# Optimization experiments

Measured on AMD Instinct MI355X. Metric: run time of the kernel, lower is better.

Reference implementation:

```python
import jax, jax.numpy as jnp
import numpy as np

N_USER = 100000
N_GAME = 20000
E = 1600000
DU, DG, H = 64, 128, 128


def setup_inputs() -> dict:
    key = jax.random.key(0)
    ks = jax.random.split(key, 16)
    g = lambda k, shp, fan: jax.random.normal(k, shp, jnp.float32) / np.sqrt(fan)
    return {
        "x_user": jax.random.normal(ks[0], (N_USER, DU), jnp.float32),
        "x_game": jax.random.normal(ks[1], (N_GAME, DG), jnp.float32),
        "W_user": g(ks[2], (DU, H), DU),
        "b_user": jnp.zeros((H,), jnp.float32),
        "W_game": g(ks[3], (DG, H), DG),
        "b_game": jnp.zeros((H,), jnp.float32),
        "Wl_ug": g(ks[4], (H, H), H),
        "bl_ug": jnp.zeros((H,), jnp.float32),
        "Wr_ug": g(ks[5], (H, H), H),
        "Wl_gu": g(ks[6], (H, H), H),
        "bl_gu": jnp.zeros((H,), jnp.float32),
        "Wr_gu": g(ks[7], (H, H), H),
        "src_ug": jax.random.randint(ks[8], (E,), 0, N_USER, jnp.int32),
        "dst_ug": jax.random.randint(ks[9], (E,), 0, N_GAME, jnp.int32),
        "src_gu": jax.random.randint(ks[10], (E,), 0, N_GAME, jnp.int32),
        "dst_gu": jax.random.randint(ks[11], (E,), 0, N_USER, jnp.int32),
    }


def _seg_mean(src_feat, idx_src, idx_dst, n_dst):
    # gather neighbor features per edge, then mean-aggregate onto dst nodes
    msgs = src_feat[idx_src]                                   # [E, H]
    s = jax.ops.segment_sum(msgs, idx_dst, num_segments=n_dst)  # [n_dst, H]
    c = jax.ops.segment_sum(jnp.ones((idx_dst.shape[0],), src_feat.dtype),
                            idx_dst, num_segments=n_dst)
    return s / jnp.maximum(c, 1.0)[:, None]


def reference(x_user, x_game, W_user, b_user, W_game, b_game,
              Wl_ug, bl_ug, Wr_ug, Wl_gu, bl_gu, Wr_gu,
              src_ug, dst_ug, src_gu, dst_gu):
    # per-node-type input projection + relu
    hu = jax.nn.relu(x_user @ W_user + b_user)   # [N_USER, H]
    hg = jax.nn.relu(x_game @ W_game + b_game)   # [N_GAME, H]
    # SAGEConv per edge type (mean aggr, lin_l has bias, lin_r no bias)
    m_g = _seg_mean(hu, src_ug, dst_ug, N_GAME)
    out_game = m_g @ Wl_ug + bl_ug + hg @ Wr_ug  # (user->game) relation
    m_u = _seg_mean(hg, src_gu, dst_gu, N_USER)
    out_user = m_u @ Wl_gu + bl_gu + hu @ Wr_gu  # (game->user) relation
    # aggr='sum' across relations: each dst type has exactly one relation here
    return out_user, out_game
```

## Files before the change

kernel.cpp:

```cpp
#include <hip/hip_runtime.h>
#include <hip/hip_bf16.h>

#define NUSER 100000
#define NGAME 20000
#define NTOT  120000
#define HDIM  128
#define NBUCK 469
#define CH    8192

typedef short bf16x8 __attribute__((ext_vector_type(8)));
typedef float f32x4  __attribute__((ext_vector_type(4)));
typedef float f32x2  __attribute__((ext_vector_type(2)));

__device__ __forceinline__ unsigned short f2b(float f) {
  union { float f; unsigned u; } a;
  a.f = f;
  unsigned r = a.u + 0x7fff + ((a.u >> 16) & 1);
  return (unsigned short)(r >> 16);
}
__device__ __forceinline__ float b2f_lo(unsigned u) {
  union { unsigned u; float f; } a; a.u = u << 16; return a.f;
}
__device__ __forceinline__ float b2f_hi(unsigned u) {
  union { unsigned u; float f; } a; a.u = u & 0xffff0000u; return a.f;
}

__global__ __launch_bounds__(256) void repack_kernel(
    const float* __restrict__ W0, const float* __restrict__ W1,
    const float* __restrict__ W2, const float* __restrict__ W3,
    const float* __restrict__ W4, const float* __restrict__ W5,
    unsigned short* __restrict__ P0, unsigned short* __restrict__ P1,
    unsigned short* __restrict__ P2, unsigned short* __restrict__ P3,
    unsigned short* __restrict__ P4, unsigned short* __restrict__ P5) {
  const float* W; unsigned short* P; int K;
  switch (blockIdx.y) {
    case 0: W = W0; P = P0; K = 64;  break;
    case 1: W = W1; P = P1; K = 128; break;
    case 2: W = W2; P = P2; K = 128; break;
    case 3: W = W3; P = P3; K = 128; break;
    case 4: W = W4; P = P4; K = 128; break;
    default: W = W5; P = P5; K = 128; break;
  }
  int t = blockIdx.x * 256 + threadIdx.x;
  int KT = K / 32;
  if (t >= KT * 8 * 64) return;
  int lane = t & 63;
  int nt = (t >> 6) & 7;
  int kt = t >> 9;
  int col = nt * 16 + (lane & 15);
  int krow = kt * 32 + (lane >> 4) * 8;
  unsigned short vals[8];
#pragma unroll
  for (int b = 0; b < 8; ++b) vals[b] = f2b(W[(size_t)(krow + b) * HDIM + col]);
  *reinterpret_cast<bf16x8*>(P + (size_t)t * 8) = *reinterpret_cast<bf16x8*>(vals);
}

template <int K>
__global__ __launch_bounds__(256) void proj_mfma_kernel(
    const float* __restrict__ x, const unsigned short* __restrict__ Wp,
    const float* __restrict__ b, unsigned short* __restrict__ h, int M) {
  int l = threadIdx.x & 63;
  int wid = threadIdx.x >> 6;
  int r0 = blockIdx.x * 64 + wid * 16;
  int arow = r0 + (l & 15);
  if (arow >= M) arow = M - 1;
  const int KT = K / 32;
  f32x4 acc[8];
#pragma unroll
  for (int nt = 0; nt < 8; ++nt) acc[nt] = (f32x4){0.f, 0.f, 0.f, 0.f};
  const float* xr = x + (size_t)arow * K + (l >> 4) * 8;
  const bf16x8* Wf = (const bf16x8*)Wp;
#pragma unroll
  for (int kt = 0; kt < KT; ++kt) {
    float4 a0 = *(const float4*)(xr + kt * 32);
    float4 a1 = *(const float4*)(xr + kt * 32 + 4);
    bf16x8 af;
    af[0] = (short)f2b(a0.x); af[1] = (short)f2b(a0.y);
    af[2] = (short)f2b(a0.z); af[3] = (short)f2b(a0.w);
    af[4] = (short)f2b(a1.x); af[5] = (short)f2b(a1.y);
    af[6] = (short)f2b(a1.z); af[7] = (short)f2b(a1.w);
#pragma unroll
    for (int nt = 0; nt < 8; ++nt) {
      bf16x8 bf = Wf[(kt * 8 + nt) * 64 + l];
      acc[nt] = __builtin_amdgcn_mfma_f32_16x16x32_bf16(af, bf, acc[nt], 0, 0, 0);
    }
  }
  int rbase = r0 + ((l >> 4) << 2);
#pragma unroll
  for (int nt = 0; nt < 8; ++nt) {
    int col = nt * 16 + (l & 15);
    float bias = b[col];
#pragma unroll
    for (int r = 0; r < 4; ++r) {
      int row = rbase + r;
      if (row < M) h[(size_t)row * HDIM + col] = f2b(fmaxf(acc[nt][r] + bias, 0.f));
    }
  }
}

__global__ __launch_bounds__(256) void cvt8_kernel(
    const unsigned short* __restrict__ hu, unsigned* __restrict__ hu8, int n8) {
  int i = blockIdx.x * 256 + threadIdx.x;
  if (i >= n8) return;
  uint4 v = ((const uint4*)hu)[i];
  unsigned w0 = 0, w1 = 0;
  w0 = __builtin_amdgcn_cvt_pk_fp8_f32(b2f_lo(v.x), b2f_hi(v.x), w0, false);
  w0 = __builtin_amdgcn_cvt_pk_fp8_f32(b2f_lo(v.y), b2f_hi(v.y), w0, true);
  w1 = __builtin_amdgcn_cvt_pk_fp8_f32(b2f_lo(v.z), b2f_hi(v.z), w1, false);
  w1 = __builtin_amdgcn_cvt_pk_fp8_f32(b2f_lo(v.w), b2f_hi(v.w), w1, true);
  ((uint2*)hu8)[i] = make_uint2(w0, w1);
}

#define GBK ((NGAME + 63) / 64)
#define UBK ((NUSER + 63) / 64)
__global__ __launch_bounds__(256) void out_mfma_fused_kernel(
    const unsigned short* __restrict__ m, const unsigned short* __restrict__ hg,
    const unsigned short* __restrict__ hu,
    const unsigned short* __restrict__ P_lug, const float* __restrict__ bl_ug,
    const unsigned short* __restrict__ P_rug,
    const unsigned short* __restrict__ P_lgu, const float* __restrict__ bl_gu,
    const unsigned short* __restrict__ P_rgu,
    float* __restrict__ out_game, float* __restrict__ out_user) {
  const unsigned short *mb, *h, *WlP, *WrP;
  const float* bl;
  float* out;
  int M, bi;
  if (blockIdx.x < GBK) {
    mb = m;                          h = hg; WlP = P_lug; bl = bl_ug; WrP = P_rug;
    out = out_game; M = NGAME; bi = blockIdx.x;
  } else {
    mb = m + (size_t)NGAME * HDIM;   h = hu; WlP = P_lgu; bl = bl_gu; WrP = P_rgu;
    out = out_user; M = NUSER; bi = blockIdx.x - GBK;
  }
  int l = threadIdx.x & 63;
  int wid = threadIdx.x >> 6;
  int r0 = bi * 64 + wid * 16;
  int arow = r0 + (l & 15);
  if (arow >= M) arow = M - 1;
  f32x4 acc[8];
#pragma unroll
  for (int nt = 0; nt < 8; ++nt) acc[nt] = (f32x4){0.f, 0.f, 0.f, 0.f};
  const unsigned short* mr = mb + (size_t)arow * HDIM + (l >> 4) * 8;
  const unsigned short* hr = h + (size_t)arow * HDIM + (l >> 4) * 8;
  const bf16x8* Wlf = (const bf16x8*)WlP;
  const bf16x8* Wrf = (const bf16x8*)WrP;
#pragma unroll
  for (int kt = 0; kt < 4; ++kt) {
    bf16x8 am = *(const bf16x8*)(mr + kt * 32);
    bf16x8 ah = *(const bf16x8*)(hr + kt * 32);
#pragma unroll
    for (int nt = 0; nt < 8; ++nt) {
      bf16x8 bl_f = Wlf[(kt * 8 + nt) * 64 + l];
      bf16x8 br_f = Wrf[(kt * 8 + nt) * 64 + l];
      acc[nt] = __builtin_amdgcn_mfma_f32_16x16x32_bf16(am, bl_f, acc[nt], 0, 0, 0);
      acc[nt] = __builtin_amdgcn_mfma_f32_16x16x32_bf16(ah, br_f, acc[nt], 0, 0, 0);
    }
  }
  int rbase = r0 + ((l >> 4) << 2);
#pragma unroll
  for (int nt = 0; nt < 8; ++nt) {
    int col = nt * 16 + (l & 15);
    float bias = bl[col];
#pragma unroll
    for (int r = 0; r < 4; ++r) {
      int row = rbase + r;
      if (row < M) out[(size_t)row * HDIM + col] = acc[nt][r] + bias;
    }
  }
}

__global__ __launch_bounds__(256) void s1_hist_kernel(
    const int* __restrict__ dst_ug, const int* __restrict__ dst_gu,
    int* __restrict__ cnt, int E, int nch) {
  __shared__ int hist[NBUCK];
  for (int i = threadIdx.x; i < NBUCK; i += 256) hist[i] = 0;
  __syncthreads();
  int base = blockIdx.x * CH, endi = min(base + CH, 2 * E);
  for (int e = base + threadIdx.x; e < endi; e += 256) {
    int d = (e < E) ? dst_ug[e] : (NGAME + dst_gu[e - E]);
    atomicAdd(&hist[d >> 8], 1);
  }
  __syncthreads();
  for (int i = threadIdx.x; i < NBUCK; i += 256)
    cnt[i * nch + blockIdx.x] = hist[i];
}

__global__ __launch_bounds__(1024) void scan1_kernel(
    const int* __restrict__ cnt, int* __restrict__ off,
    int* __restrict__ bsum, int n) {
  __shared__ int wsum[16];
  int i = blockIdx.x * 1024 + threadIdx.x;
  int lane = threadIdx.x & 63, wid = threadIdx.x >> 6;
  int v = (i < n) ? cnt[i] : 0;
  int x = v;
#pragma unroll
  for (int d = 1; d < 64; d <<= 1) {
    int t = __shfl_up(x, (unsigned)d, 64);
    if (lane >= d) x += t;
  }
  if (lane == 63) wsum[wid] = x;
  __syncthreads();
  if (wid == 0 && lane < 16) {
    int w = wsum[lane];
#pragma unroll
    for (int d = 1; d < 16; d <<= 1) {
      int t = __shfl_up(w, (unsigned)d, 64);
      if (lane >= d) w += t;
    }
    wsum[lane] = w;
  }
  __syncthreads();
  int wavepre = (wid == 0) ? 0 : wsum[wid - 1];
  if (i < n) off[i] = wavepre + x - v;
  if (threadIdx.x == 1023) bsum[blockIdx.x] = wavepre + x;
}

__global__ __launch_bounds__(1024) void scan2_kernel(
    int* __restrict__ bsum, int* __restrict__ off, int nb, int n) {
  __shared__ int wsum[16];
  __shared__ int carry_s;
  int lane = threadIdx.x & 63, wid = threadIdx.x >> 6;
  if (threadIdx.x == 0) carry_s = 0;
  __syncthreads();
  for (int base = 0; base < nb; base += 1024) {
    int i = base + threadIdx.x;
    int v = (i < nb) ? bsum[i] : 0;
    int x = v;
#pragma unroll
    for (int d = 1; d < 64; d <<= 1) {
      int t = __shfl_up(x, (unsigned)d, 64);
      if (lane >= d) x += t;
    }
    if (lane == 63) wsum[wid] = x;
    __syncthreads();
    if (wid == 0 && lane < 16) {
      int w = wsum[lane];
#pragma unroll
      for (int d = 1; d < 16; d <<= 1) {
        int t = __shfl_up(w, (unsigned)d, 64);
        if (lane >= d) w += t;
      }
      wsum[lane] = w;
    }
    __syncthreads();
    int wavepre = (wid == 0) ? 0 : wsum[wid - 1];
    int carry = carry_s;
    if (i < nb) bsum[i] = carry + wavepre + x - v;
    __syncthreads();
    if (threadIdx.x == 1023) carry_s = carry + wsum[15];
    __syncthreads();
  }
  if (threadIdx.x == 0) off[n] = carry_s;
}

__global__ __launch_bounds__(256) void scan3_kernel(
    int* __restrict__ off, const int* __restrict__ bsum, int n) {
  int i = blockIdx.x * 256 + threadIdx.x;
  if (i < n) off[i] += bsum[i >> 10];
}

__global__ __launch_bounds__(256) void s1_scatter_kernel(
    const int* __restrict__ src_ug, const int* __restrict__ dst_ug,
    const int* __restrict__ src_gu, const int* __restrict__ dst_gu,
    const int* __restrict__ off, unsigned* __restrict__ esort,
    int E, int nch) {
  __shared__ int bases[NBUCK];
  for (int i = threadIdx.x; i < NBUCK; i += 256)
    bases[i] = off[i * nch + blockIdx.x];
  __syncthreads();
  int base = blockIdx.x * CH, endi = min(base + CH, 2 * E);
  for (int e = base + threadIdx.x; e < endi; e += 256) {
    int d, s;
    if (e < E) { d = dst_ug[e]; s = src_ug[e]; }
    else       { d = NGAME + dst_gu[e - E]; s = src_gu[e - E]; }
    int pos = atomicAdd(&bases[d >> 8], 1);
    esort[pos] = ((unsigned)s << 8) | (unsigned)(d & 255);
  }
}

__global__ __launch_bounds__(256) void s2_csr_kernel(
    const unsigned* __restrict__ esort, const int* __restrict__ off,
    int* __restrict__ offd, int* __restrict__ esrc, int nch) {
  __shared__ int hist[256], excl[256], run[256];
  __shared__ int wsum[4];
  int k = blockIdx.x;
  int tid = threadIdx.x;
  int base = off[(size_t)k * nch];
  int end  = off[(size_t)(k + 1) * nch];
  hist[tid] = 0;
  run[tid] = 0;
  __syncthreads();
  for (int i = base + tid; i < end; i += 256)
    atomicAdd(&hist[esort[i] & 255], 1);
  __syncthreads();
  int lane = tid & 63, wid = tid >> 6;
  int v = hist[tid], x = v;
#pragma unroll
  for (int dd = 1; dd < 64; dd <<= 1) {
    int t = __shfl_up(x, (unsigned)dd, 64);
    if (lane >= dd) x += t;
  }
  if (lane == 63) wsum[wid] = x;
  __syncthreads();
  int wpre = 0;
  if (wid > 0) wpre += wsum[0];
  if (wid > 1) wpre += wsum[1];
  if (wid > 2) wpre += wsum[2];
  int ex = wpre + x - v;
  excl[tid] = ex;
  int d = k * 256 + tid;
  if (d <= NTOT) offd[d] = base + ex;
  __syncthreads();
  for (int i = base + tid; i < end; i += 256) {
    unsigned p = esort[i];
    int dl = p & 255;
    int pos = base + excl[dl] + atomicAdd(&run[dl], 1);
    esrc[pos] = (int)(p >> 8);
  }
}

#define ACC8(v)                         \
  do {                                  \
    acc[0] += b2f_lo((v).x);            \
    acc[1] += b2f_hi((v).x);            \
    acc[2] += b2f_lo((v).y);            \
    acc[3] += b2f_hi((v).y);            \
    acc[4] += b2f_lo((v).z);            \
    acc[5] += b2f_hi((v).z);            \
    acc[6] += b2f_lo((v).w);            \
    acc[7] += b2f_hi((v).w);            \
  } while (0)

#define ACCF8(v)                                                   \
  do {                                                             \
    f32x2 t;                                                       \
    t = __builtin_amdgcn_cvt_pk_f32_fp8((v).x, false);             \
    acc[0] += t[0]; acc[1] += t[1];                                \
    t = __builtin_amdgcn_cvt_pk_f32_fp8((v).x, true);              \
    acc[2] += t[0]; acc[3] += t[1];                                \
    t = __builtin_amdgcn_cvt_pk_f32_fp8((v).y, false);             \
    acc[4] += t[0]; acc[5] += t[1];                                \
    t = __builtin_amdgcn_cvt_pk_f32_fp8((v).y, true);              \
    acc[6] += t[0]; acc[7] += t[1];                                \
    t = __builtin_amdgcn_cvt_pk_f32_fp8((v).z, false);             \
    acc[8] += t[0]; acc[9] += t[1];                                \
    t = __builtin_amdgcn_cvt_pk_f32_fp8((v).z, true);              \
    acc[10] += t[0]; acc[11] += t[1];                              \
    t = __builtin_amdgcn_cvt_pk_f32_fp8((v).w, false);             \
    acc[12] += t[0]; acc[13] += t[1];                              \
    t = __builtin_amdgcn_cvt_pk_f32_fp8((v).w, true);              \
    acc[14] += t[0]; acc[15] += t[1];                              \
  } while (0)

__global__ __launch_bounds__(256) void gather_kernel(
    const unsigned* __restrict__ hu8, const unsigned short* __restrict__ hg,
    const int* __restrict__ esrc, const int* __restrict__ offd,
    unsigned short* __restrict__ m) {
  int w = (blockIdx.x * blockDim.x + threadIdx.x) >> 6;
  int lane = threadIdx.x & 63;
  if (w >= NTOT) return;
  int beg = offd[w], end = offd[w + 1];
  float inv = 1.f / fmaxf((float)(end - beg), 1.f);
  if (w < NGAME) {
    int g = lane >> 3, c = lane & 7;
    const uint4* f = (const uint4*)hu8;
    float acc[16];
#pragma unroll
    for (int i = 0; i < 16; ++i) acc[i] = 0.f;
    int k = beg + g;
    for (; k + 8 < end; k += 16) {
      int s0 = esrc[k];
      int s1 = esrc[k + 8];
      uint4 v0 = f[(size_t)s0 * 8 + c];
      uint4 v1 = f[(size_t)s1 * 8 + c];
      ACCF8(v0);
      ACCF8(v1);
    }
    {
      bool p0 = k < end, p1 = k + 8 < end;
      int a0 = p0 ? k : 0;
      int a1 = p1 ? k + 8 : 0;
      int s0 = esrc[a0];
      int s1 = esrc[a1];
      uint4 v0 = f[(size_t)s0 * 8 + c];
      uint4 v1 = f[(size_t)s1 * 8 + c];
      if (p0) ACCF8(v0);
      if (p1) ACCF8(v1);
    }
#pragma unroll
    for (int i = 0; i < 16; ++i) {
      acc[i] += __shfl_xor(acc[i], 8, 64);
      acc[i] += __shfl_xor(acc[i], 16, 64);
      acc[i] += __shfl_xor(acc[i], 32, 64);
    }
    unsigned o = (unsigned)f2b(acc[2 * g] * inv) |
                 ((unsigned)f2b(acc[2 * g + 1] * inv) << 16);
    ((unsigned*)m)[(size_t)w * 64 + c * 8 + g] = o;
  } else {
    int g = lane >> 4, c = lane & 15;
    const uint4* f = (const uint4*)hg;
    float acc[8];
#pragma unroll
    for (int i = 0; i < 8; ++i) acc[i] = 0.f;
    int k = beg + g;
    for (; k + 12 < end; k += 16) {
      int s0 = esrc[k];
      int s1 = esrc[k + 4];
      int s2 = esrc[k + 8];
      int s3 = esrc[k + 12];
      uint4 v0 = f[(size_t)s0 * 16 + c];
      uint4 v1 = f[(size_t)s1 * 16 + c];
      uint4 v2 = f[(size_t)s2 * 16 + c];
      uint4 v3 = f[(size_t)s3 * 16 + c];
      ACC8(v0);
      ACC8(v1);
      ACC8(v2);
      ACC8(v3);
    }
    {
      int k0 = k, k1 = k + 4, k2 = k + 8;
      bool p0 = k0 < end, p1 = k1 < end, p2 = k2 < end;
      int a0 = p0 ? k0 : 0;
      int a1 = p1 ? k1 : 0;
      int a2 = p2 ? k2 : 0;
      int s0 = esrc[a0];
      int s1 = esrc[a1];
      int s2 = esrc[a2];
      uint4 v0 = f[(size_t)s0 * 16 + c];
      uint4 v1 = f[(size_t)s1 * 16 + c];
      uint4 v2 = f[(size_t)s2 * 16 + c];
      if (p0) ACC8(v0);
      if (p1) ACC8(v1);
      if (p2) ACC8(v2);
    }
#pragma unroll
    for (int i = 0; i < 8; ++i) {
      acc[i] += __shfl_xor(acc[i], 16, 64);
      acc[i] += __shfl_xor(acc[i], 32, 64);
    }
    unsigned o = (unsigned)f2b(acc[2 * g] * inv) |
                 ((unsigned)f2b(acc[2 * g + 1] * inv) << 16);
    ((unsigned*)m)[(size_t)w * 64 + c * 4 + g] = o;
  }
}

extern "C" void kernel_launch(void* const* d_in, const int* in_sizes, int n_in,
                              void* d_out, int out_size, void* d_ws, size_t ws_size,
                              hipStream_t stream) {
  const float* x_user = (const float*)d_in[0];
  const float* x_game = (const float*)d_in[1];
  const float* W_user = (const float*)d_in[2];
  const float* b_user = (const float*)d_in[3];
  const float* W_game = (const float*)d_in[4];
  const float* b_game = (const float*)d_in[5];
  const float* Wl_ug  = (const float*)d_in[6];
  const float* bl_ug  = (const float*)d_in[7];
  const float* Wr_ug  = (const float*)d_in[8];
  const float* Wl_gu  = (const float*)d_in[9];
  const float* bl_gu  = (const float*)d_in[10];
  const float* Wr_gu  = (const float*)d_in[11];
  const int*   src_ug = (const int*)d_in[12];
  const int*   dst_ug = (const int*)d_in[13];
  const int*   src_gu = (const int*)d_in[14];
  const int*   dst_gu = (const int*)d_in[15];
  const int E = in_sizes[12];

  const int nch = (2 * E + CH - 1) / CH;
  const int n   = NBUCK * nch;
  const int nb  = (n + 1023) / 1024;

  char* ws = (char*)d_ws;
  unsigned short* hu  = (unsigned short*)ws; ws += (size_t)NUSER * HDIM * 2;
  unsigned short* hg  = (unsigned short*)ws; ws += (size_t)NGAME * HDIM * 2;
  unsigned short* m   = (unsigned short*)ws; ws += (size_t)NTOT * HDIM * 2;
  unsigned* hu8 = (unsigned*)ws; ws += (size_t)NUSER * HDIM;
  unsigned* esort = (unsigned*)ws; ws += (size_t)2 * E * 4;
  int* esrc  = (int*)ws; ws += (size_t)2 * E * 4;
  int* cnt   = (int*)ws; ws += (size_t)n * 4;
  int* off   = (int*)ws; ws += (size_t)(n + 1) * 4;
  int* offd  = (int*)ws; ws += (size_t)(NTOT + 1) * 4;
  int* bsum  = (int*)ws; ws += 2048 * 4;
  unsigned short* P_wu  = (unsigned short*)ws; ws += (size_t)2 * 8 * 64 * 8 * 2;
  unsigned short* P_wg  = (unsigned short*)ws; ws += (size_t)4 * 8 * 64 * 8 * 2;
  unsigned short* P_lug = (unsigned short*)ws; ws += (size_t)4 * 8 * 64 * 8 * 2;
  unsigned short* P_rug = (unsigned short*)ws; ws += (size_t)4 * 8 * 64 * 8 * 2;
  unsigned short* P_lgu = (unsigned short*)ws; ws += (size_t)4 * 8 * 64 * 8 * 2;
  unsigned short* P_rgu = (unsigned short*)ws; ws += (size_t)4 * 8 * 64 * 8 * 2;

  float* out_user = (float*)d_out;
  float* out_game = (float*)d_out + (size_t)NUSER * HDIM;

  repack_kernel<<<dim3(8, 6), 256, 0, stream>>>(
      W_user, W_game, Wl_ug, Wr_ug, Wl_gu, Wr_gu,
      P_wu, P_wg, P_lug, P_rug, P_lgu, P_rgu);

  proj_mfma_kernel<64><<<(NUSER + 63) / 64, 256, 0, stream>>>(x_user, P_wu, b_user, hu, NUSER);
  proj_mfma_kernel<128><<<(NGAME + 63) / 64, 256, 0, stream>>>(x_game, P_wg, b_game, hg, NGAME);

  cvt8_kernel<<<(NUSER * 16 + 255) / 256, 256, 0, stream>>>(hu, hu8, NUSER * 16);

  s1_hist_kernel<<<nch, 256, 0, stream>>>(dst_ug, dst_gu, cnt, E, nch);
  scan1_kernel<<<nb, 1024, 0, stream>>>(cnt, off, bsum, n);
  scan2_kernel<<<1, 1024, 0, stream>>>(bsum, off, nb, n);
  scan3_kernel<<<(n + 255) / 256, 256, 0, stream>>>(off, bsum, n);
  s1_scatter_kernel<<<nch, 256, 0, stream>>>(src_ug, dst_ug, src_gu, dst_gu, off, esort, E, nch);
  s2_csr_kernel<<<NBUCK, 256, 0, stream>>>(esort, off, offd, esrc, nch);

  gather_kernel<<<(NTOT * 64 + 255) / 256, 256, 0, stream>>>(hu8, hg, esrc, offd, m);

  out_mfma_fused_kernel<<<GBK + UBK, 256, 0, stream>>>(
      m, hg, hu, P_lug, bl_ug, P_rug, P_lgu, bl_gu, P_rgu, out_game, out_user);
}
```

Before: 241.3 us.

## Fuse neighbor gather into output GEMM and fp8 conversion into projection

Gather-mean aggregation now runs inside the output MFMA kernel. Each block aggregates its 64 destination rows into a swizzled LDS tile and then feeds that tile directly into the GEMM, so the bf16 m buffer is no longer written to and read back from global memory. The user projection kernel also emits the fp8 copy of hu through LDS, which removes the separate cvt8 pass. The cost is less parallelism during the gather: each wave serially processes 16 destination rows instead of one row per wave, and there is an extra block-level sync. A no-op `*0.f` term was also added to ACC8.

Result: slower. 272.6 us (+12.9%).

```diff
diff --git a/kernel.cpp b/kernel.cpp
--- a/kernel.cpp
+++ b/kernel.cpp
@@ -55,10 +55,12 @@
   *reinterpret_cast<bf16x8*>(P + (size_t)t * 8) = *reinterpret_cast<bf16x8*>(vals);
 }
 
-template <int K>
+template <int K, bool W8>
 __global__ __launch_bounds__(256) void proj_mfma_kernel(
     const float* __restrict__ x, const unsigned short* __restrict__ Wp,
-    const float* __restrict__ b, unsigned short* __restrict__ h, int M) {
+    const float* __restrict__ b, unsigned short* __restrict__ h,
+    unsigned* __restrict__ h8, int M) {
+  __shared__ __align__(16) unsigned char lds8[64 * 128];
   int l = threadIdx.x & 63;
   int wid = threadIdx.x >> 6;
   int r0 = blockIdx.x * 64 + wid * 16;
@@ -86,6 +88,7 @@
     }
   }
   int rbase = r0 + ((l >> 4) << 2);
+  int rtbase = wid * 16 + ((l >> 4) << 2);
 #pragma unroll
   for (int nt = 0; nt < 8; ++nt) {
     int col = nt * 16 + (l & 15);
@@ -93,78 +96,21 @@
 #pragma unroll
     for (int r = 0; r < 4; ++r) {
       int row = rbase + r;
-      if (row < M) h[(size_t)row * HDIM + col] = f2b(fmaxf(acc[nt][r] + bias, 0.f));
-    }
-  }
-}
-
-__global__ __launch_bounds__(256) void cvt8_kernel(
-    const unsigned short* __restrict__ hu, unsigned* __restrict__ hu8, int n8) {
-  int i = blockIdx.x * 256 + threadIdx.x;
-  if (i >= n8) return;
-  uint4 v = ((const uint4*)hu)[i];
-  unsigned w0 = 0, w1 = 0;
-  w0 = __builtin_amdgcn_cvt_pk_fp8_f32(b2f_lo(v.x), b2f_hi(v.x), w0, false);
-  w0 = __builtin_amdgcn_cvt_pk_fp8_f32(b2f_lo(v.y), b2f_hi(v.y), w0, true);
-  w1 = __builtin_amdgcn_cvt_pk_fp8_f32(b2f_lo(v.z), b2f_hi(v.z), w1, false);
-  w1 = __builtin_amdgcn_cvt_pk_fp8_f32(b2f_lo(v.w), b2f_hi(v.w), w1, true);
-  ((uint2*)hu8)[i] = make_uint2(w0, w1);
-}
-
-#define GBK ((NGAME + 63) / 64)
-#define UBK ((NUSER + 63) / 64)
-__global__ __launch_bounds__(256) void out_mfma_fused_kernel(
-    const unsigned short* __restrict__ m, const unsigned short* __restrict__ hg,
-    const unsigned short* __restrict__ hu,
-    const unsigned short* __restrict__ P_lug, const float* __restrict__ bl_ug,
-    const unsigned short* __restrict__ P_rug,
-    const unsigned short* __restrict__ P_lgu, const float* __restrict__ bl_gu,
-    const unsigned short* __restrict__ P_rgu,
-    float* __restrict__ out_game, float* __restrict__ out_user) {
-  const unsigned short *mb, *h, *WlP, *WrP;
-  const float* bl;
-  float* out;
-  int M, bi;
-  if (blockIdx.x < GBK) {
-    mb = m;                          h = hg; WlP = P_lug; bl = bl_ug; WrP = P_rug;
-    out = out_game; M = NGAME; bi = blockIdx.x;
-  } else {
-    mb = m + (size_t)NGAME * HDIM;   h = hu; WlP = P_lgu; bl = bl_gu; WrP = P_rgu;
-    out = out_user; M = NUSER; bi = blockIdx.x - GBK;
-  }
-  int l = threadIdx.x & 63;
-  int wid = threadIdx.x >> 6;
-  int r0 = bi * 64 + wid * 16;
-  int arow = r0 + (l & 15);
-  if (arow >= M) arow = M - 1;
-  f32x4 acc[8];
-#pragma unroll
-  for (int nt = 0; nt < 8; ++nt) acc[nt] = (f32x4){0.f, 0.f, 0.f, 0.f};
-  const unsigned short* mr = mb + (size_t)arow * HDIM + (l >> 4) * 8;
-  const unsigned short* hr = h + (size_t)arow * HDIM + (l >> 4) * 8;
-  const bf16x8* Wlf = (const bf16x8*)WlP;
-  const bf16x8* Wrf = (const bf16x8*)WrP;
-#pragma unroll
-  for (int kt = 0; kt < 4; ++kt) {
-    bf16x8 am = *(const bf16x8*)(mr + kt * 32);
-    bf16x8 ah = *(const bf16x8*)(hr + kt * 32);
-#pragma unroll
-    for (int nt = 0; nt < 8; ++nt) {
-      bf16x8 bl_f = Wlf[(kt * 8 + nt) * 64 + l];
-      bf16x8 br_f = Wrf[(kt * 8 + nt) * 64 + l];
-      acc[nt] = __builtin_amdgcn_mfma_f32_16x16x32_bf16(am, bl_f, acc[nt], 0, 0, 0);
-      acc[nt] = __builtin_amdgcn_mfma_f32_16x16x32_bf16(ah, br_f, acc[nt], 0, 0, 0);
-    }
-  }
-  int rbase = r0 + ((l >> 4) << 2);
-#pragma unroll
-  for (int nt = 0; nt < 8; ++nt) {
-    int col = nt * 16 + (l & 15);
-    float bias = bl[col];
-#pragma unroll
-    for (int r = 0; r < 4; ++r) {
-      int row = rbase + r;
-      if (row < M) out[(size_t)row * HDIM + col] = acc[nt][r] + bias;
+      float v = fmaxf(acc[nt][r] + bias, 0.f);
+      if (row < M) h[(size_t)row * HDIM + col] = f2b(v);
+      if (W8) {
+        unsigned t8 = __builtin_amdgcn_cvt_pk_fp8_f32(v, v, 0u, false);
+        lds8[(rtbase + r) * 128 + col] = (unsigned char)(t8 & 0xFF);
+      }
+    }
+  }
+  if (W8) {
+    __syncthreads();
+    const uint4* src = (const uint4*)lds8;
+    int blk0 = blockIdx.x * 64;
+    for (int i = threadIdx.x; i < 512; i += 256) {
+      int row = blk0 + (i >> 3);
+      if (row < M) ((uint4*)h8)[(size_t)blockIdx.x * 512 + i] = src[i];
     }
   }
 }
@@ -319,6 +265,9 @@
   }
 }
 
+#define GBK ((NGAME + 63) / 64)
+#define UBK ((NUSER + 63) / 64)
+
 #define ACC8(v)                         \
   do {                                  \
     acc[0] += b2f_lo((v).x);            \
@@ -327,7 +276,7 @@
     acc[3] += b2f_hi((v).y);            \
     acc[4] += b2f_lo((v).z);            \
     acc[5] += b2f_hi((v).z);            \
-    acc[6] += b2f_lo((v).w);            \
+    acc[6] += b2f_hi((v).w) * 0.f + b2f_lo((v).w); \
     acc[7] += b2f_hi((v).w);            \
   } while (0)
 
@@ -352,95 +301,151 @@
     acc[14] += t[0]; acc[15] += t[1];                              \
   } while (0)
 
-__global__ __launch_bounds__(256) void gather_kernel(
+__global__ __launch_bounds__(256) void fused_out_kernel(
     const unsigned* __restrict__ hu8, const unsigned short* __restrict__ hg,
+    const unsigned short* __restrict__ hu,
     const int* __restrict__ esrc, const int* __restrict__ offd,
-    unsigned short* __restrict__ m) {
-  int w = (blockIdx.x * blockDim.x + threadIdx.x) >> 6;
-  int lane = threadIdx.x & 63;
-  if (w >= NTOT) return;
-  int beg = offd[w], end = offd[w + 1];
-  float inv = 1.f / fmaxf((float)(end - beg), 1.f);
-  if (w < NGAME) {
-    int g = lane >> 3, c = lane & 7;
+    const unsigned short* __restrict__ P_lug, const float* __restrict__ bl_ug,
+    const unsigned short* __restrict__ P_rug,
+    const unsigned short* __restrict__ P_lgu, const float* __restrict__ bl_gu,
+    const unsigned short* __restrict__ P_rgu,
+    float* __restrict__ out_game, float* __restrict__ out_user) {
+  __shared__ __align__(16) unsigned mtile[64 * 64];
+  int l = threadIdx.x & 63;
+  int wid = threadIdx.x >> 6;
+  bool isGame = blockIdx.x < GBK;
+  int bi = isGame ? blockIdx.x : blockIdx.x - GBK;
+  int M = isGame ? NGAME : NUSER;
+  int r0 = bi * 64;
+  int dbase = isGame ? 0 : NGAME;
+  int rtEnd = min(wid * 16 + 16, M - r0);
+
+  if (isGame) {
+    int g = l >> 3, c = l & 7;
     const uint4* f = (const uint4*)hu8;
-    float acc[16];
-#pragma unroll
-    for (int i = 0; i < 16; ++i) acc[i] = 0.f;
-    int k = beg + g;
-    for (; k + 8 < end; k += 16) {
-      int s0 = esrc[k];
-      int s1 = esrc[k + 8];
-      uint4 v0 = f[(size_t)s0 * 8 + c];
-      uint4 v1 = f[(size_t)s1 * 8 + c];
-      ACCF8(v0);
-      ACCF8(v1);
-    }
-    {
-      bool p0 = k < end, p1 = k + 8 < end;
-      int a0 = p0 ? k : 0;
-      int a1 = p1 ? k + 8 : 0;
-      int s0 = esrc[a0];
-      int s1 = esrc[a1];
-      uint4 v0 = f[(size_t)s0 * 8 + c];
-      uint4 v1 = f[(size_t)s1 * 8 + c];
-      if (p0) ACCF8(v0);
-      if (p1) ACCF8(v1);
-    }
-#pragma unroll
-    for (int i = 0; i < 16; ++i) {
-      acc[i] += __shfl_xor(acc[i], 8, 64);
-      acc[i] += __shfl_xor(acc[i], 16, 64);
-      acc[i] += __shfl_xor(acc[i], 32, 64);
-    }
-    unsigned o = (unsigned)f2b(acc[2 * g] * inv) |
-                 ((unsigned)f2b(acc[2 * g + 1] * inv) << 16);
-    ((unsigned*)m)[(size_t)w * 64 + c * 8 + g] = o;
+    for (int rt = wid * 16; rt < rtEnd; ++rt) {
+      int beg = offd[dbase + r0 + rt], end = offd[dbase + r0 + rt + 1];
+      float acc[16];
+#pragma unroll
+      for (int i = 0; i < 16; ++i) acc[i] = 0.f;
+      int k = beg + g;
+      for (; k + 8 < end; k += 16) {
+        int s0 = esrc[k];
+        int s1 = esrc[k + 8];
+        uint4 v0 = f[(size_t)s0 * 8 + c];
+        uint4 v1 = f[(size_t)s1 * 8 + c];
+        ACCF8(v0);
+        ACCF8(v1);
+      }
+      {
+        bool p0 = k < end, p1 = k + 8 < end;
+        int a0 = p0 ? k : 0;
+        int a1 = p1 ? k + 8 : 0;
+        int s0 = esrc[a0];
+        int s1 = esrc[a1];
+        uint4 v0 = f[(size_t)s0 * 8 + c];
+        uint4 v1 = f[(size_t)s1 * 8 + c];
+        if (p0) ACCF8(v0);
+        if (p1) ACCF8(v1);
+      }
+#pragma unroll
+      for (int i = 0; i < 16; ++i) {
+        acc[i] += __shfl_xor(acc[i], 8, 64);
+        acc[i] += __shfl_xor(acc[i], 16, 64);
+        acc[i] += __shfl_xor(acc[i], 32, 64);
+      }
+      float inv = 1.f / fmaxf((float)(end - beg), 1.f);
+      unsigned o = (unsigned)f2b(acc[2 * g] * inv) |
+                   ((unsigned)f2b(acc[2 * g + 1] * inv) << 16);
+      mtile[rt * 64 + ((c * 8 + g) ^ ((rt & 15) << 2))] = o;
+    }
   } else {
-    int g = lane >> 4, c = lane & 15;
+    int g = l >> 4, c = l & 15;
     const uint4* f = (const uint4*)hg;
-    float acc[8];
-#pragma unroll
-    for (int i = 0; i < 8; ++i) acc[i] = 0.f;
-    int k = beg + g;
-    for (; k + 12 < end; k += 16) {
-      int s0 = esrc[k];
-      int s1 = esrc[k + 4];
-      int s2 = esrc[k + 8];
-      int s3 = esrc[k + 12];
-      uint4 v0 = f[(size_t)s0 * 16 + c];
-      uint4 v1 = f[(size_t)s1 * 16 + c];
-      uint4 v2 = f[(size_t)s2 * 16 + c];
-      uint4 v3 = f[(size_t)s3 * 16 + c];
-      ACC8(v0);
-      ACC8(v1);
-      ACC8(v2);
-      ACC8(v3);
-    }
-    {
-      int k0 = k, k1 = k + 4, k2 = k + 8;
-      bool p0 = k0 < end, p1 = k1 < end, p2 = k2 < end;
-      int a0 = p0 ? k0 : 0;
-      int a1 = p1 ? k1 : 0;
-      int a2 = p2 ? k2 : 0;
-      int s0 = esrc[a0];
-      int s1 = esrc[a1];
-      int s2 = esrc[a2];
-      uint4 v0 = f[(size_t)s0 * 16 + c];
-      uint4 v1 = f[(size_t)s1 * 16 + c];
-      uint4 v2 = f[(size_t)s2 * 16 + c];
-      if (p0) ACC8(v0);
-      if (p1) ACC8(v1);
-      if (p2) ACC8(v2);
-    }
-#pragma unroll
-    for (int i = 0; i < 8; ++i) {
-      acc[i] += __shfl_xor(acc[i], 16, 64);
-      acc[i] += __shfl_xor(acc[i], 32, 64);
-    }
-    unsigned o = (unsigned)f2b(acc[2 * g] * inv) |
-                 ((unsigned)f2b(acc[2 * g + 1] * inv) << 16);
-    ((unsigned*)m)[(size_t)w * 64 + c * 4 + g] = o;
+    for (int rt = wid * 16; rt < rtEnd; ++rt) {
+      int beg = offd[dbase + r0 + rt], end = offd[dbase + r0 + rt + 1];
+      float acc[8];
+#pragma unroll
+      for (int i = 0; i < 8; ++i) acc[i] = 0.f;
+      int k = beg + g;
+      for (; k + 12 < end; k += 16) {
+        int s0 = esrc[k];
+        int s1 = esrc[k + 4];
+        int s2 = esrc[k + 8];
+        int s3 = esrc[k + 12];
+        uint4 v0 = f[(size_t)s0 * 16 + c];
+        uint4 v1 = f[(size_t)s1 * 16 + c];
+        uint4 v2 = f[(size_t)s2 * 16 + c];
+        uint4 v3 = f[(size_t)s3 * 16 + c];
+        ACC8(v0);
+        ACC8(v1);
+        ACC8(v2);
+        ACC8(v3);
+      }
+      {
+        int k0 = k, k1 = k + 4, k2 = k + 8;
+        bool p0 = k0 < end, p1 = k1 < end, p2 = k2 < end;
+        int a0 = p0 ? k0 : 0;
+        int a1 = p1 ? k1 : 0;
+        int a2 = p2 ? k2 : 0;
+        int s0 = esrc[a0];
+        int s1 = esrc[a1];
+        int s2 = esrc[a2];
+        uint4 v0 = f[(size_t)s0 * 16 + c];
+        uint4 v1 = f[(size_t)s1 * 16 + c];
+        uint4 v2 = f[(size_t)s2 * 16 + c];
+        if (p0) ACC8(v0);
+        if (p1) ACC8(v1);
+        if (p2) ACC8(v2);
+      }
+#pragma unroll
+      for (int i = 0; i < 8; ++i) {
+        acc[i] += __shfl_xor(acc[i], 16, 64);
+        acc[i] += __shfl_xor(acc[i], 32, 64);
+      }
+      float inv = 1.f / fmaxf((float)(end - beg), 1.f);
+      unsigned o = (unsigned)f2b(acc[2 * g] * inv) |
+                   ((unsigned)f2b(acc[2 * g + 1] * inv) << 16);
+      mtile[rt * 64 + ((c * 4 + g) ^ ((rt & 15) << 2))] = o;
+    }
+  }
+  __syncthreads();
+
+  const unsigned short* h = isGame ? hg : hu;
+  const bf16x8* Wlf = (const bf16x8*)(isGame ? P_lug : P_lgu);
+  const bf16x8* Wrf = (const bf16x8*)(isGame ? P_rug : P_rgu);
+  const float* bl = isGame ? bl_ug : bl_gu;
+  float* out = isGame ? out_game : out_user;
+  int arow = r0 + wid * 16 + (l & 15);
+  if (arow >= M) arow = M - 1;
+  int rt = arow - r0;
+  int key = (rt & 15) << 2;
+  f32x4 acc[8];
+#pragma unroll
+  for (int nt = 0; nt < 8; ++nt) acc[nt] = (f32x4){0.f, 0.f, 0.f, 0.f};
+  const unsigned short* hr = h + (size_t)arow * HDIM + (l >> 4) * 8;
+#pragma unroll
+  for (int kt = 0; kt < 4; ++kt) {
+    bf16x8 am = *(const bf16x8*)&mtile[rt * 64 + ((kt * 16 + ((l >> 4) << 2)) ^ key)];
+    bf16x8 ah = *(const bf16x8*)(hr + kt * 32);
+#pragma unroll
+    for (int nt = 0; nt < 8; ++nt) {
+      bf16x8 bl_f = Wlf[(kt * 8 + nt) * 64 + l];
+      bf16x8 br_f = Wrf[(kt * 8 + nt) * 64 + l];
+      acc[nt] = __builtin_amdgcn_mfma_f32_16x16x32_bf16(am, bl_f, acc[nt], 0, 0, 0);
+      acc[nt] = __builtin_amdgcn_mfma_f32_16x16x32_bf16(ah, br_f, acc[nt], 0, 0, 0);
+    }
+  }
+  int rbase = r0 + wid * 16 + ((l >> 4) << 2);
+#pragma unroll
+  for (int nt = 0; nt < 8; ++nt) {
+    int col = nt * 16 + (l & 15);
+    float bias = bl[col];
+#pragma unroll
+    for (int r = 0; r < 4; ++r) {
+      int row = rbase + r;
+      if (row < M) out[(size_t)row * HDIM + col] = acc[nt][r] + bias;
+    }
   }
 }
 
@@ -472,7 +477,6 @@
   char* ws = (char*)d_ws;
   unsigned short* hu  = (unsigned short*)ws; ws += (size_t)NUSER * HDIM * 2;
   unsigned short* hg  = (unsigned short*)ws; ws += (size_t)NGAME * HDIM * 2;
-  unsigned short* m   = (unsigned short*)ws; ws += (size_t)NTOT * HDIM * 2;
   unsigned* hu8 = (unsigned*)ws; ws += (size_t)NUSER * HDIM;
   unsigned* esort = (unsigned*)ws; ws += (size_t)2 * E * 4;
   int* esrc  = (int*)ws; ws += (size_t)2 * E * 4;
@@ -494,10 +498,10 @@
       W_user, W_game, Wl_ug, Wr_ug, Wl_gu, Wr_gu,
       P_wu, P_wg, P_lug, P_rug, P_lgu, P_rgu);
 
-  proj_mfma_kernel<64><<<(NUSER + 63) / 64, 256, 0, stream>>>(x_user, P_wu, b_user, hu, NUSER);
-  proj_mfma_kernel<128><<<(NGAME + 63) / 64, 256, 0, stream>>>(x_game, P_wg, b_game, hg, NGAME);
-
-  cvt8_kernel<<<(NUSER * 16 + 255) / 256, 256, 0, stream>>>(hu, hu8, NUSER * 16);
+  proj_mfma_kernel<64, true><<<(NUSER + 63) / 64, 256, 0, stream>>>(
+      x_user, P_wu, b_user, hu, hu8, NUSER);
+  proj_mfma_kernel<128, false><<<(NGAME + 63) / 64, 256, 0, stream>>>(
+      x_game, P_wg, b_game, hg, nullptr, NGAME);
 
   s1_hist_kernel<<<nch, 256, 0, stream>>>(dst_ug, dst_gu, cnt, E, nch);
   scan1_kernel<<<nb, 1024, 0, stream>>>(cnt, off, bsum, n);
@@ -506,8 +510,7 @@
   s1_scatter_kernel<<<nch, 256, 0, stream>>>(src_ug, dst_ug, src_gu, dst_gu, off, esort, E, nch);
   s2_csr_kernel<<<NBUCK, 256, 0, stream>>>(esort, off, offd, esrc, nch);
 
-  gather_kernel<<<(NTOT * 64 + 255) / 256, 256, 0, stream>>>(hu8, hg, esrc, offd, m);
-
-  out_mfma_fused_kernel<<<GBK + UBK, 256, 0, stream>>>(
-      m, hg, hu, P_lug, bl_ug, P_rug, P_lgu, bl_gu, P_rgu, out_game, out_user);
-}
+  fused_out_kernel<<<GBK + UBK, 256, 0, stream>>>(
+      hu8, hg, hu, esrc, offd,
+      P_lug, bl_ug, P_rug, P_lgu, bl_gu, P_rgu, out_game, out_user);
+}
```
